# Kernel optimization log

Hardware: AMD Instinct MI355X
Metric: run time of the kernel (lower is better)

## Reference

```python
import jax, jax.numpy as jnp
import numpy as np

B, S, E = 8, 2048, 512
VOCAB, FVOCAB = 32000, 128
SCALE = float(np.power(E, 0.5))  # emb_size ** (0.5 * temper), temper=1


def setup_inputs() -> dict:
    key = jax.random.key(0)
    ks = jax.random.split(key, 7)
    key_seq = jax.random.randint(ks[0], (B, S), 0, VOCAB, dtype=jnp.int32)
    value_seq = jax.random.randint(ks[1], (B, S), 0, FVOCAB, dtype=jnp.int32)
    hidden = jax.random.normal(ks[2], (B, S, E), dtype=jnp.float32)
    mask_matrix = jax.random.uniform(ks[3], (B, S, S), dtype=jnp.float32)
    nan_matrix = jnp.zeros((1,), dtype=jnp.int32)  # unused by forward
    # learned params; padding_idx=0 -> zero row in embeddings
    key_emb = jax.random.normal(ks[4], (VOCAB, E), dtype=jnp.float32).at[0].set(0.0)
    value_emb = jax.random.normal(ks[5], (FVOCAB, E), dtype=jnp.float32).at[0].set(0.0)
    weight = jax.random.normal(ks[6], (E, E), dtype=jnp.float32) / np.sqrt(E)
    return {
        "key_seq": key_seq, "value_seq": value_seq, "hidden": hidden,
        "mask_matrix": mask_matrix, "nan_matrix": nan_matrix,
        "key_emb": key_emb, "value_emb": value_emb, "weight": weight,
    }


def reference(key_seq, value_seq, hidden, mask_matrix, nan_matrix,
              key_emb, value_emb, weight):
    k = key_emb[key_seq]          # [B,S,E]
    v = value_emb[value_seq]      # [B,S,E]
    q = jnp.einsum('bsd,de->bse', hidden, weight)   # hidden @ weight
    u = jnp.einsum('bse,bte->bst', q, k) / SCALE    # QK^T, [B,S,S]
    mask = jnp.clip(mask_matrix.astype(u.dtype), 0.0, 1.0)
    exp_u = jnp.exp(u)
    delta = exp_u * mask
    p = delta / (jnp.sum(delta, axis=2, keepdims=True) + 1e-10)
    o = jnp.einsum('bst,bte->bse', p, v)            # PV, [B,S,E]
    return o
```

## Files before the change

kernel.cpp:

```cpp
#include <hip/hip_runtime.h>
#include <stdint.h>

#define BB 8
#define SS 2048
#define EE 512
#define INV_SCALE 0.04419417382415922f

typedef __attribute__((ext_vector_type(8))) short bf8_t;
typedef __attribute__((ext_vector_type(4))) float f4_t;

__device__ __forceinline__ unsigned short f2bf(float f) {
    union { float f; uint32_t u; } x; x.f = f;
    uint32_t r = x.u + 0x7fffu + ((x.u >> 16) & 1u);
    return (unsigned short)(r >> 16);
}

__device__ __forceinline__ float bfbits2f(uint32_t hi_bits) {
    union { uint32_t u; float f; } x; x.u = hi_bits;
    return x.f;
}


__global__ void __launch_bounds__(256) gather_k_kernel(const int* __restrict__ idx,
                                                       const float* __restrict__ emb,
                                                       unsigned short* __restrict__ out) {
    int id = blockIdx.x * 256 + threadIdx.x;
    int chunk = id & 63;
    int row = id >> 6;
    int e0 = chunk * 8;
    int k = idx[row];
    const float* src = emb + (size_t)k * EE + e0;
    float4 a = *(const float4*)(src);
    float4 c = *(const float4*)(src + 4);
    union { unsigned short s[8]; int4 v; } u;
    u.s[0] = f2bf(a.x); u.s[1] = f2bf(a.y); u.s[2] = f2bf(a.z); u.s[3] = f2bf(a.w);
    u.s[4] = f2bf(c.x); u.s[5] = f2bf(c.y); u.s[6] = f2bf(c.z); u.s[7] = f2bf(c.w);
    *(int4*)(out + (size_t)row * EE + e0) = u.v;
}

__global__ void __launch_bounds__(256) cast_h_kernel(const float* __restrict__ in,
                                                     unsigned short* __restrict__ out) {
    int id = blockIdx.x * 256 + threadIdx.x;
    const float* src = in + (size_t)id * 8;
    float4 a = *(const float4*)(src);
    float4 c = *(const float4*)(src + 4);
    union { unsigned short s[8]; int4 v; } u;
    u.s[0] = f2bf(a.x); u.s[1] = f2bf(a.y); u.s[2] = f2bf(a.z); u.s[3] = f2bf(a.w);
    u.s[4] = f2bf(c.x); u.s[5] = f2bf(c.y); u.s[6] = f2bf(c.z); u.s[7] = f2bf(c.w);
    *(int4*)(out + (size_t)id * 8) = u.v;
}

__global__ void __launch_bounds__(256) gather_vt_kernel(const int* __restrict__ idx,
                                                        const float* __restrict__ emb,
                                                        unsigned short* __restrict__ vt) {
    int id = blockIdx.x * 256 + threadIdx.x;
    int t8 = id & 255;
    int rest = id >> 8;
    int e = rest & (EE - 1);
    int b = rest >> 9;
    int t0 = t8 * 8;
    const int* ip = idx + b * SS + t0;
    int4 i0 = *(const int4*)(ip);
    int4 i1 = *(const int4*)(ip + 4);
    union { unsigned short s[8]; int4 v; } u;
    u.s[0] = f2bf(emb[(size_t)i0.x * EE + e]);
    u.s[1] = f2bf(emb[(size_t)i0.y * EE + e]);
    u.s[2] = f2bf(emb[(size_t)i0.z * EE + e]);
    u.s[3] = f2bf(emb[(size_t)i0.w * EE + e]);
    u.s[4] = f2bf(emb[(size_t)i1.x * EE + e]);
    u.s[5] = f2bf(emb[(size_t)i1.y * EE + e]);
    u.s[6] = f2bf(emb[(size_t)i1.z * EE + e]);
    u.s[7] = f2bf(emb[(size_t)i1.w * EE + e]);
    *(int4*)(vt + ((size_t)b * EE + e) * SS + t0) = u.v;
}

__global__ void __launch_bounds__(256) transpose_w_kernel(const float* __restrict__ w,
                                                          unsigned short* __restrict__ wt) {
    int id = blockIdx.x * 256 + threadIdx.x;
    int e = id & (EE - 1);
    int f = id >> 9;
    wt[id] = f2bf(w[(size_t)e * EE + f] * INV_SCALE);
}


__device__ __forceinline__ void stage_tile64(const unsigned short* gbase, int ld, int k0,
                                             unsigned short* lds, int wave, int lane) {
#pragma unroll
    for (int i = 0; i < 4; ++i) {
        int row = i * 32 + wave * 8 + (lane >> 3);
        int col = (lane & 7) * 8;
        const unsigned short* g = gbase + (size_t)row * ld + (k0 + col);
        unsigned short* l = lds + i * 2048 + wave * 512 + lane * 8;
        __builtin_amdgcn_global_load_lds((const __attribute__((address_space(1))) unsigned int*)g,
                                         (__attribute__((address_space(3))) unsigned int*)l,
                                         16, 0, 0);
    }
}

template <int KLEN>
__device__ __forceinline__ void mfma_loop(const unsigned short* Abase, int lda,
                                          const unsigned short* Bbase, int ldb,
                                          unsigned short* As, unsigned short* Bs,
                                          f4_t acc[4][4], int wave, int lane) {
    const int wm = wave >> 1, wn = wave & 1;
    const int quad = lane >> 4, l16 = lane & 15;
#pragma unroll 1
    for (int k0 = 0; k0 < KLEN; k0 += 64) {
        stage_tile64(Abase, lda, k0, As, wave, lane);
        stage_tile64(Bbase, ldb, k0, Bs, wave, lane);
        __syncthreads();
#pragma unroll
        for (int kk = 0; kk < 2; ++kk) {
            bf8_t af[4], bfr[4];
#pragma unroll
            for (int mi = 0; mi < 4; ++mi)
                af[mi] = *(const bf8_t*)(As + (wm * 64 + mi * 16 + l16) * 64 + kk * 32 + quad * 8);
#pragma unroll
            for (int ni = 0; ni < 4; ++ni)
                bfr[ni] = *(const bf8_t*)(Bs + (wn * 64 + ni * 16 + l16) * 64 + kk * 32 + quad * 8);
#pragma unroll
            for (int mi = 0; mi < 4; ++mi)
#pragma unroll
                for (int ni = 0; ni < 4; ++ni)
                    acc[mi][ni] = __builtin_amdgcn_mfma_f32_16x16x32_bf16(af[mi], bfr[ni],
                                                                          acc[mi][ni], 0, 0, 0);
        }
        __syncthreads();
    }
}


__global__ void __launch_bounds__(256) qgen_kernel(const unsigned short* __restrict__ H,
                                                   const unsigned short* __restrict__ Wt,
                                                   unsigned short* __restrict__ Q) {
    __shared__ unsigned short As[128 * 64];
    __shared__ unsigned short Bs[128 * 64];
    const int tid = threadIdx.x, wave = tid >> 6, lane = tid & 63;
    const int rowT = blockIdx.y;
    const int colT = blockIdx.x;
    f4_t acc[4][4];
    const f4_t z = {0.f, 0.f, 0.f, 0.f};
    for (int i = 0; i < 4; ++i) for (int j = 0; j < 4; ++j) acc[i][j] = z;
    mfma_loop<EE>(H + (size_t)rowT * 128 * EE, EE,
                  Wt + (size_t)colT * 128 * EE, EE, As, Bs, acc, wave, lane);
    const int wm = wave >> 1, wn = wave & 1, quad = lane >> 4, l16 = lane & 15;
#pragma unroll
    for (int mi = 0; mi < 4; ++mi)
#pragma unroll
        for (int r = 0; r < 4; ++r) {
            int row = rowT * 128 + wm * 64 + mi * 16 + quad * 4 + r;
#pragma unroll
            for (int ni = 0; ni < 4; ++ni) {
                int col = colT * 128 + wn * 64 + ni * 16 + l16;
                Q[(size_t)row * EE + col] = f2bf(acc[mi][ni][r]);
            }
        }
}

__global__ void __launch_bounds__(256) qk_kernel(const unsigned short* __restrict__ Q,
                                                 const unsigned short* __restrict__ K,
                                                 const float* __restrict__ mask,
                                                 unsigned short* __restrict__ delta,
                                                 float* __restrict__ lsum) {
    __shared__ unsigned short As[128 * 64];
    __shared__ unsigned short Bs[128 * 64];
    const int tid = threadIdx.x, wave = tid >> 6, lane = tid & 63;
    const int b = blockIdx.z, qT = blockIdx.y, tT = blockIdx.x;
    const int wm = wave >> 1, wn = wave & 1, quad = lane >> 4, l16 = lane & 15;

    uint32_t mpk[4][4][2];
#pragma unroll
    for (int mi = 0; mi < 4; ++mi)
#pragma unroll
        for (int r = 0; r < 4; ++r) {
            int row = qT * 128 + wm * 64 + mi * 16 + quad * 4 + r;
            const float* mrow = mask + ((size_t)b * SS + row) * SS;
#pragma unroll
            for (int h = 0; h < 2; ++h) {
                float m0 = mrow[tT * 128 + wn * 64 + (2 * h) * 16 + l16];
                float m1 = mrow[tT * 128 + wn * 64 + (2 * h + 1) * 16 + l16];
                m0 = fminf(fmaxf(m0, 0.f), 1.f);
                m1 = fminf(fmaxf(m1, 0.f), 1.f);
                mpk[mi][r][h] = (uint32_t)f2bf(m0) | ((uint32_t)f2bf(m1) << 16);
            }
        }

    f4_t acc[4][4];
    const f4_t z = {0.f, 0.f, 0.f, 0.f};
    for (int i = 0; i < 4; ++i) for (int j = 0; j < 4; ++j) acc[i][j] = z;
    mfma_loop<EE>(Q + ((size_t)b * SS + qT * 128) * EE, EE,
                  K + ((size_t)b * SS + tT * 128) * EE, EE, As, Bs, acc, wave, lane);

#pragma unroll
    for (int mi = 0; mi < 4; ++mi)
#pragma unroll
        for (int r = 0; r < 4; ++r) {
            int row = qT * 128 + wm * 64 + mi * 16 + quad * 4 + r;
            unsigned short* drow = delta + ((size_t)b * SS + row) * SS;
            float psum = 0.f;
#pragma unroll
            for (int h = 0; h < 2; ++h) {
                uint32_t pk = mpk[mi][r][h];
                float mlo = bfbits2f(pk << 16);
                float mhi = bfbits2f(pk & 0xffff0000u);
                int col0 = tT * 128 + wn * 64 + (2 * h) * 16 + l16;
                int col1 = col0 + 16;
                float e0 = __expf(acc[mi][2 * h][r]) * mlo;
                float e1 = __expf(acc[mi][2 * h + 1][r]) * mhi;
                drow[col0] = f2bf(e0);
                drow[col1] = f2bf(e1);
                psum += e0 + e1;
            }
#pragma unroll
            for (int off = 1; off < 16; off <<= 1)
                psum += __shfl_xor(psum, off, 16);
            if (l16 == 0) atomicAdd(&lsum[b * SS + row], psum);
        }
}

__global__ void __launch_bounds__(256) pv_kernel(const unsigned short* __restrict__ delta,
                                                 const unsigned short* __restrict__ Vt,
                                                 const float* __restrict__ lsum,
                                                 float* __restrict__ out) {
    __shared__ unsigned short As[128 * 64];
    __shared__ unsigned short Bs[128 * 64];
    const int tid = threadIdx.x, wave = tid >> 6, lane = tid & 63;
    const int b = blockIdx.z, qT = blockIdx.y, eT = blockIdx.x;
    const int wm = wave >> 1, wn = wave & 1, quad = lane >> 4, l16 = lane & 15;

    float inv[4][4];
#pragma unroll
    for (int mi = 0; mi < 4; ++mi)
#pragma unroll
        for (int r = 0; r < 4; ++r) {
            int row = qT * 128 + wm * 64 + mi * 16 + quad * 4 + r;
            inv[mi][r] = lsum[b * SS + row];
        }
#pragma unroll
    for (int mi = 0; mi < 4; ++mi)
#pragma unroll
        for (int r = 0; r < 4; ++r)
            inv[mi][r] = 1.0f / (inv[mi][r] + 1e-10f);

    f4_t acc[4][4];
    const f4_t z = {0.f, 0.f, 0.f, 0.f};
    for (int i = 0; i < 4; ++i) for (int j = 0; j < 4; ++j) acc[i][j] = z;
    mfma_loop<SS>(delta + ((size_t)b * SS + qT * 128) * SS, SS,
                  Vt + ((size_t)b * EE + eT * 128) * SS, SS, As, Bs, acc, wave, lane);

#pragma unroll
    for (int mi = 0; mi < 4; ++mi)
#pragma unroll
        for (int r = 0; r < 4; ++r) {
            int row = qT * 128 + wm * 64 + mi * 16 + quad * 4 + r;
#pragma unroll
            for (int ni = 0; ni < 4; ++ni) {
                int col = eT * 128 + wn * 64 + ni * 16 + l16;
                out[((size_t)b * SS + row) * EE + col] = acc[mi][ni][r] * inv[mi][r];
            }
        }
}


extern "C" void kernel_launch(void* const* d_in, const int* in_sizes, int n_in,
                              void* d_out, int out_size, void* d_ws, size_t ws_size,
                              hipStream_t stream) {
    const int*   key_seq = (const int*)d_in[0];
    const int*   val_seq = (const int*)d_in[1];
    const float* hidden  = (const float*)d_in[2];
    const float* mask    = (const float*)d_in[3];
    const float* key_emb = (const float*)d_in[5];
    const float* val_emb = (const float*)d_in[6];
    const float* weight  = (const float*)d_in[7];
    float* out = (float*)d_out;

    char* ws = (char*)d_ws;
    const size_t SZ_BSE = (size_t)BB * SS * EE * sizeof(unsigned short);
    unsigned short* Q    = (unsigned short*)(ws);
    unsigned short* K    = (unsigned short*)(ws + SZ_BSE);
    unsigned short* Vt   = (unsigned short*)(ws + 2 * SZ_BSE);
    unsigned short* H    = (unsigned short*)(ws + 3 * SZ_BSE);
    unsigned short* Wt   = (unsigned short*)(ws + 4 * SZ_BSE);
    float*          lsum = (float*)(ws + 4 * SZ_BSE + 524288);
    unsigned short* delta= (unsigned short*)(ws + 4 * SZ_BSE + 524288 + 65536);

    hipMemsetAsync(lsum, 0, (size_t)BB * SS * sizeof(float), stream);

    gather_k_kernel<<<4096, 256, 0, stream>>>(key_seq, key_emb, K);
    cast_h_kernel<<<4096, 256, 0, stream>>>(hidden, H);
    gather_vt_kernel<<<4096, 256, 0, stream>>>(val_seq, val_emb, Vt);
    transpose_w_kernel<<<1024, 256, 0, stream>>>(weight, Wt);

    qgen_kernel<<<dim3(4, 128), 256, 0, stream>>>(H, Wt, Q);
    qk_kernel<<<dim3(16, 16, 8), 256, 0, stream>>>(Q, K, mask, delta, lsum);
    pv_kernel<<<dim3(4, 16, 8), 256, 0, stream>>>(delta, Vt, lsum, out);
}
```

Baseline: 480.1 us.

## Widen QK and PV output tiles to 256 columns and halve the K-step to 32

The QK and PV kernels now compute 128x256 output tiles per block, with 4x8 accumulators per wave, so each staged A tile is reused across twice as many columns. The K-loop step drops from 64 to 32, which halves the LDS footprint but doubles the number of barriers per reduction. The mask reads in QK move from before the matmul loop to the epilogue, so they no longer overlap with the MFMA work. The PV grid shrinks to 256 blocks, which risks lower occupancy and weaker latency hiding.

Result: slower. 505.0 us (+5.2%).

```diff
diff --git a/kernel.cpp b/kernel.cpp
--- a/kernel.cpp
+++ b/kernel.cpp
@@ -13,11 +13,6 @@
     union { float f; uint32_t u; } x; x.f = f;
     uint32_t r = x.u + 0x7fffu + ((x.u >> 16) & 1u);
     return (unsigned short)(r >> 16);
-}
-
-__device__ __forceinline__ float bfbits2f(uint32_t hi_bits) {
-    union { uint32_t u; float f; } x; x.u = hi_bits;
-    return x.f;
 }
 
 
@@ -82,13 +77,13 @@
     wt[id] = f2bf(w[(size_t)e * EE + f] * INV_SCALE);
 }
 
-
-__device__ __forceinline__ void stage_tile64(const unsigned short* gbase, int ld, int k0,
+template <int NPASS>
+__device__ __forceinline__ void stage_tile32(const unsigned short* gbase, int ld, int k0,
                                              unsigned short* lds, int wave, int lane) {
 #pragma unroll
-    for (int i = 0; i < 4; ++i) {
-        int row = i * 32 + wave * 8 + (lane >> 3);
-        int col = (lane & 7) * 8;
+    for (int i = 0; i < NPASS; ++i) {
+        int row = i * 64 + wave * 16 + (lane >> 2);
+        int col = (lane & 3) * 8;
         const unsigned short* g = gbase + (size_t)row * ld + (k0 + col);
         unsigned short* l = lds + i * 2048 + wave * 512 + lane * 8;
         __builtin_amdgcn_global_load_lds((const __attribute__((address_space(1))) unsigned int*)g,
@@ -98,33 +93,59 @@
 }
 
 template <int KLEN>
-__device__ __forceinline__ void mfma_loop(const unsigned short* Abase, int lda,
-                                          const unsigned short* Bbase, int ldb,
-                                          unsigned short* As, unsigned short* Bs,
-                                          f4_t acc[4][4], int wave, int lane) {
+__device__ __forceinline__ void mfma_loop_128(const unsigned short* Abase, int lda,
+                                              const unsigned short* Bbase, int ldb,
+                                              unsigned short* As, unsigned short* Bs,
+                                              f4_t acc[4][4], int wave, int lane) {
     const int wm = wave >> 1, wn = wave & 1;
     const int quad = lane >> 4, l16 = lane & 15;
 #pragma unroll 1
-    for (int k0 = 0; k0 < KLEN; k0 += 64) {
-        stage_tile64(Abase, lda, k0, As, wave, lane);
-        stage_tile64(Bbase, ldb, k0, Bs, wave, lane);
+    for (int k0 = 0; k0 < KLEN; k0 += 32) {
+        stage_tile32<2>(Abase, lda, k0, As, wave, lane);
+        stage_tile32<2>(Bbase, ldb, k0, Bs, wave, lane);
         __syncthreads();
-#pragma unroll
-        for (int kk = 0; kk < 2; ++kk) {
-            bf8_t af[4], bfr[4];
-#pragma unroll
-            for (int mi = 0; mi < 4; ++mi)
-                af[mi] = *(const bf8_t*)(As + (wm * 64 + mi * 16 + l16) * 64 + kk * 32 + quad * 8);
+        bf8_t af[4], bfr[4];
+#pragma unroll
+        for (int mi = 0; mi < 4; ++mi)
+            af[mi] = *(const bf8_t*)(As + (wm * 64 + mi * 16 + l16) * 32 + quad * 8);
+#pragma unroll
+        for (int ni = 0; ni < 4; ++ni)
+            bfr[ni] = *(const bf8_t*)(Bs + (wn * 64 + ni * 16 + l16) * 32 + quad * 8);
+#pragma unroll
+        for (int mi = 0; mi < 4; ++mi)
 #pragma unroll
             for (int ni = 0; ni < 4; ++ni)
-                bfr[ni] = *(const bf8_t*)(Bs + (wn * 64 + ni * 16 + l16) * 64 + kk * 32 + quad * 8);
-#pragma unroll
-            for (int mi = 0; mi < 4; ++mi)
-#pragma unroll
-                for (int ni = 0; ni < 4; ++ni)
-                    acc[mi][ni] = __builtin_amdgcn_mfma_f32_16x16x32_bf16(af[mi], bfr[ni],
-                                                                          acc[mi][ni], 0, 0, 0);
-        }
+                acc[mi][ni] = __builtin_amdgcn_mfma_f32_16x16x32_bf16(af[mi], bfr[ni],
+                                                                      acc[mi][ni], 0, 0, 0);
+        __syncthreads();
+    }
+}
+
+template <int KLEN>
+__device__ __forceinline__ void mfma_loop_wide(const unsigned short* Abase, int lda,
+                                               const unsigned short* Bbase, int ldb,
+                                               unsigned short* As, unsigned short* Bs,
+                                               f4_t acc[4][8], int wave, int lane) {
+    const int wm = wave >> 1, wn = wave & 1;
+    const int quad = lane >> 4, l16 = lane & 15;
+#pragma unroll 1
+    for (int k0 = 0; k0 < KLEN; k0 += 32) {
+        stage_tile32<2>(Abase, lda, k0, As, wave, lane);
+        stage_tile32<4>(Bbase, ldb, k0, Bs, wave, lane);
+        __syncthreads();
+        bf8_t af[4], bfr[8];
+#pragma unroll
+        for (int mi = 0; mi < 4; ++mi)
+            af[mi] = *(const bf8_t*)(As + (wm * 64 + mi * 16 + l16) * 32 + quad * 8);
+#pragma unroll
+        for (int ni = 0; ni < 8; ++ni)
+            bfr[ni] = *(const bf8_t*)(Bs + (wn * 128 + ni * 16 + l16) * 32 + quad * 8);
+#pragma unroll
+        for (int mi = 0; mi < 4; ++mi)
+#pragma unroll
+            for (int ni = 0; ni < 8; ++ni)
+                acc[mi][ni] = __builtin_amdgcn_mfma_f32_16x16x32_bf16(af[mi], bfr[ni],
+                                                                      acc[mi][ni], 0, 0, 0);
         __syncthreads();
     }
 }
@@ -133,16 +154,16 @@
 __global__ void __launch_bounds__(256) qgen_kernel(const unsigned short* __restrict__ H,
                                                    const unsigned short* __restrict__ Wt,
                                                    unsigned short* __restrict__ Q) {
-    __shared__ unsigned short As[128 * 64];
-    __shared__ unsigned short Bs[128 * 64];
+    __shared__ unsigned short As[128 * 32];
+    __shared__ unsigned short Bs[128 * 32];
     const int tid = threadIdx.x, wave = tid >> 6, lane = tid & 63;
     const int rowT = blockIdx.y;
     const int colT = blockIdx.x;
     f4_t acc[4][4];
     const f4_t z = {0.f, 0.f, 0.f, 0.f};
     for (int i = 0; i < 4; ++i) for (int j = 0; j < 4; ++j) acc[i][j] = z;
-    mfma_loop<EE>(H + (size_t)rowT * 128 * EE, EE,
-                  Wt + (size_t)colT * 128 * EE, EE, As, Bs, acc, wave, lane);
+    mfma_loop_128<EE>(H + (size_t)rowT * 128 * EE, EE,
+                      Wt + (size_t)colT * 128 * EE, EE, As, Bs, acc, wave, lane);
     const int wm = wave >> 1, wn = wave & 1, quad = lane >> 4, l16 = lane & 15;
 #pragma unroll
     for (int mi = 0; mi < 4; ++mi)
@@ -162,54 +183,37 @@
                                                  const float* __restrict__ mask,
                                                  unsigned short* __restrict__ delta,
                                                  float* __restrict__ lsum) {
-    __shared__ unsigned short As[128 * 64];
-    __shared__ unsigned short Bs[128 * 64];
+    __shared__ unsigned short As[128 * 32];
+    __shared__ unsigned short Bs[256 * 32];
     const int tid = threadIdx.x, wave = tid >> 6, lane = tid & 63;
     const int b = blockIdx.z, qT = blockIdx.y, tT = blockIdx.x;
     const int wm = wave >> 1, wn = wave & 1, quad = lane >> 4, l16 = lane & 15;
 
-    uint32_t mpk[4][4][2];
+    f4_t acc[4][8];
+    const f4_t z = {0.f, 0.f, 0.f, 0.f};
+    for (int i = 0; i < 4; ++i) for (int j = 0; j < 8; ++j) acc[i][j] = z;
+    mfma_loop_wide<EE>(Q + ((size_t)b * SS + qT * 128) * EE, EE,
+                       K + ((size_t)b * SS + tT * 256) * EE, EE, As, Bs, acc, wave, lane);
+
 #pragma unroll
     for (int mi = 0; mi < 4; ++mi)
 #pragma unroll
         for (int r = 0; r < 4; ++r) {
             int row = qT * 128 + wm * 64 + mi * 16 + quad * 4 + r;
             const float* mrow = mask + ((size_t)b * SS + row) * SS;
-#pragma unroll
-            for (int h = 0; h < 2; ++h) {
-                float m0 = mrow[tT * 128 + wn * 64 + (2 * h) * 16 + l16];
-                float m1 = mrow[tT * 128 + wn * 64 + (2 * h + 1) * 16 + l16];
-                m0 = fminf(fmaxf(m0, 0.f), 1.f);
-                m1 = fminf(fmaxf(m1, 0.f), 1.f);
-                mpk[mi][r][h] = (uint32_t)f2bf(m0) | ((uint32_t)f2bf(m1) << 16);
-            }
-        }
-
-    f4_t acc[4][4];
-    const f4_t z = {0.f, 0.f, 0.f, 0.f};
-    for (int i = 0; i < 4; ++i) for (int j = 0; j < 4; ++j) acc[i][j] = z;
-    mfma_loop<EE>(Q + ((size_t)b * SS + qT * 128) * EE, EE,
-                  K + ((size_t)b * SS + tT * 128) * EE, EE, As, Bs, acc, wave, lane);
-
-#pragma unroll
-    for (int mi = 0; mi < 4; ++mi)
-#pragma unroll
-        for (int r = 0; r < 4; ++r) {
-            int row = qT * 128 + wm * 64 + mi * 16 + quad * 4 + r;
             unsigned short* drow = delta + ((size_t)b * SS + row) * SS;
+            float mv[8];
+#pragma unroll
+            for (int ni = 0; ni < 8; ++ni)
+                mv[ni] = mrow[tT * 256 + wn * 128 + ni * 16 + l16];
             float psum = 0.f;
 #pragma unroll
-            for (int h = 0; h < 2; ++h) {
-                uint32_t pk = mpk[mi][r][h];
-                float mlo = bfbits2f(pk << 16);
-                float mhi = bfbits2f(pk & 0xffff0000u);
-                int col0 = tT * 128 + wn * 64 + (2 * h) * 16 + l16;
-                int col1 = col0 + 16;
-                float e0 = __expf(acc[mi][2 * h][r]) * mlo;
-                float e1 = __expf(acc[mi][2 * h + 1][r]) * mhi;
-                drow[col0] = f2bf(e0);
-                drow[col1] = f2bf(e1);
-                psum += e0 + e1;
+            for (int ni = 0; ni < 8; ++ni) {
+                float m = fminf(fmaxf(mv[ni], 0.f), 1.f);
+                float e = __expf(acc[mi][ni][r]) * m;
+                int col = tT * 256 + wn * 128 + ni * 16 + l16;
+                drow[col] = f2bf(e);
+                psum += e;
             }
 #pragma unroll
             for (int off = 1; off < 16; off <<= 1)
@@ -222,8 +226,8 @@
                                                  const unsigned short* __restrict__ Vt,
                                                  const float* __restrict__ lsum,
                                                  float* __restrict__ out) {
-    __shared__ unsigned short As[128 * 64];
-    __shared__ unsigned short Bs[128 * 64];
+    __shared__ unsigned short As[128 * 32];
+    __shared__ unsigned short Bs[256 * 32];
     const int tid = threadIdx.x, wave = tid >> 6, lane = tid & 63;
     const int b = blockIdx.z, qT = blockIdx.y, eT = blockIdx.x;
     const int wm = wave >> 1, wn = wave & 1, quad = lane >> 4, l16 = lane & 15;
@@ -242,11 +246,11 @@
         for (int r = 0; r < 4; ++r)
             inv[mi][r] = 1.0f / (inv[mi][r] + 1e-10f);
 
-    f4_t acc[4][4];
+    f4_t acc[4][8];
     const f4_t z = {0.f, 0.f, 0.f, 0.f};
-    for (int i = 0; i < 4; ++i) for (int j = 0; j < 4; ++j) acc[i][j] = z;
-    mfma_loop<SS>(delta + ((size_t)b * SS + qT * 128) * SS, SS,
-                  Vt + ((size_t)b * EE + eT * 128) * SS, SS, As, Bs, acc, wave, lane);
+    for (int i = 0; i < 4; ++i) for (int j = 0; j < 8; ++j) acc[i][j] = z;
+    mfma_loop_wide<SS>(delta + ((size_t)b * SS + qT * 128) * SS, SS,
+                       Vt + ((size_t)b * EE + eT * 256) * SS, SS, As, Bs, acc, wave, lane);
 
 #pragma unroll
     for (int mi = 0; mi < 4; ++mi)
@@ -254,8 +258,8 @@
         for (int r = 0; r < 4; ++r) {
             int row = qT * 128 + wm * 64 + mi * 16 + quad * 4 + r;
 #pragma unroll
-            for (int ni = 0; ni < 4; ++ni) {
-                int col = eT * 128 + wn * 64 + ni * 16 + l16;
+            for (int ni = 0; ni < 8; ++ni) {
+                int col = eT * 256 + wn * 128 + ni * 16 + l16;
                 out[((size_t)b * SS + row) * EE + col] = acc[mi][ni][r] * inv[mi][r];
             }
         }
@@ -292,6 +296,6 @@
     transpose_w_kernel<<<1024, 256, 0, stream>>>(weight, Wt);
 
     qgen_kernel<<<dim3(4, 128), 256, 0, stream>>>(H, Wt, Q);
-    qk_kernel<<<dim3(16, 16, 8), 256, 0, stream>>>(Q, K, mask, delta, lsum);
-    pv_kernel<<<dim3(4, 16, 8), 256, 0, stream>>>(delta, Vt, lsum, out);
-}
+    qk_kernel<<<dim3(8, 16, 8), 256, 0, stream>>>(Q, K, mask, delta, lsum);
+    pv_kernel<<<dim3(2, 16, 8), 256, 0, stream>>>(delta, Vt, lsum, out);
+}
```
